# Kernel optimization log

Measured on AMD Instinct MI355X. Metric: run time of the kernel, lower is better.

Reference implementation:

```python
import jax, jax.numpy as jnp
import numpy as np
from jax.scipy.linalg import expm

B, HW, SPP, C, H, W = 4, 16384, 3, 64, 128, 128
D_SH = 25
EPS = 1e-8

# color SH mask: higher degrees downweighted (from GaussianAdapter.__init__)
_SH_MASK = np.ones(D_SH, np.float32)
for _d in range(1, 5):
    _SH_MASK[_d * _d:(_d + 1) * (_d + 1)] = 0.1 * 0.25 ** _d

# --- e3nn-style SO(3) generators for wigner_D (precomputed in numpy) ---

def _su2_generators(j):
    m = np.arange(-j, j)
    raising = np.diag(-np.sqrt(j * (j + 1) - m * (m + 1)), k=-1).astype(np.complex128)
    m = np.arange(-j + 1, j + 1)
    lowering = np.diag(np.sqrt(j * (j + 1) - m * (m - 1)), k=1).astype(np.complex128)
    m = np.arange(-j, j + 1)
    return np.stack([0.5 * (raising + lowering), np.diag(1j * m), -0.5j * (raising - lowering)])

def _change_basis(l):
    q = np.zeros((2 * l + 1, 2 * l + 1), dtype=np.complex128)
    for m in range(-l, 0):
        q[l + m, l + abs(m)] = 1 / np.sqrt(2)
        q[l + m, l - abs(m)] = -1j / np.sqrt(2)
    q[l, l] = 1.0
    for m in range(1, l + 1):
        q[l + m, l + abs(m)] = (-1) ** m / np.sqrt(2)
        q[l + m, l - abs(m)] = 1j * (-1) ** m / np.sqrt(2)
    return (-1j) ** l * q

def _so3_generators(l):
    X = _su2_generators(l)
    Q = _change_basis(l)
    return np.real(np.conj(Q.T) @ X @ Q).astype(np.float32)

_SO3 = [_so3_generators(l) for l in range(5)]

# --- small math helpers ---

def _quat_to_mat(q):  # q: (..., 4) wxyz, pytorch3d convention
    r, i, j, k = q[..., 0], q[..., 1], q[..., 2], q[..., 3]
    s = 2.0 / jnp.sum(q * q, axis=-1)
    m = jnp.stack([
        1 - s * (j * j + k * k), s * (i * j - k * r), s * (i * k + j * r),
        s * (i * j + k * r), 1 - s * (i * i + k * k), s * (j * k - i * r),
        s * (i * k - j * r), s * (j * k + i * r), 1 - s * (i * i + j * j)], -1)
    return m.reshape(q.shape[:-1] + (3, 3))

def _rot_y(a):
    c, s = jnp.cos(a), jnp.sin(a)
    z, o = jnp.zeros_like(a), jnp.ones_like(a)
    return jnp.stack([jnp.stack([c, z, s], -1), jnp.stack([z, o, z], -1), jnp.stack([-s, z, c], -1)], -2)

def _rot_x(a):
    c, s = jnp.cos(a), jnp.sin(a)
    z, o = jnp.zeros_like(a), jnp.ones_like(a)
    return jnp.stack([jnp.stack([o, z, z], -1), jnp.stack([z, c, -s], -1), jnp.stack([z, s, c], -1)], -2)

def _matrix_to_angles(R):  # e3nn matrix_to_angles, YXY convention
    x = R[..., :, 1]  # R @ e_y
    x = x / jnp.linalg.norm(x, axis=-1, keepdims=True)
    beta = jnp.arccos(jnp.clip(x[..., 1], -1.0, 1.0))
    alpha = jnp.arctan2(x[..., 0], x[..., 2])
    A = _rot_y(alpha) @ _rot_x(beta)  # angles_to_matrix(alpha, beta, 0)
    Rp = jnp.swapaxes(A, -1, -2) @ R
    gamma = jnp.arctan2(Rp[..., 0, 2], Rp[..., 0, 0])
    return alpha, beta, gamma

def _wigner_D(l, alpha, beta, gamma):  # alpha/beta/gamma: [b]
    X = jnp.asarray(_SO3[l])
    ea = jax.vmap(expm)(alpha[:, None, None] * X[1])
    eb = jax.vmap(expm)(beta[:, None, None] * X[0])
    eg = jax.vmap(expm)(gamma[:, None, None] * X[1])
    return ea @ eb @ eg  # [b, 2l+1, 2l+1]

def _rotate_sh(sh, R):  # sh: [b,hw,spp,3,25], R: [b,3,3]
    alpha, beta, gamma = _matrix_to_angles(R)
    out = []
    for l in range(5):
        D = _wigner_D(l, alpha, -beta, gamma)
        out.append(jnp.einsum('bij,bhscj->bhsci', D, sh[..., l * l:(l + 1) * (l + 1)]))
    return jnp.concatenate(out, axis=-1)

def _forward(extrinsics, intrinsics, coordinates, depths, opacities, raw_gaussians, grd_feat, image_h, image_w):
    scales_raw = raw_gaussians[..., :3]
    rot_raw = raw_gaussians[..., 3:7]
    color_sh = raw_gaussians[..., 7:7 + 3 * D_SH]
    b, c, h, w = grd_feat.shape
    features = jnp.transpose(grd_feat.reshape(b, c, h * w), (0, 2, 1))[:, :, None, :]  # [b,hw,1,c]
    scales = 0.5 + (15.0 - 0.5) * jax.nn.sigmoid(scales_raw)
    pixel_size = jnp.array([1.0 / image_w, 1.0 / image_h], dtype=jnp.float32)
    K2inv = jnp.linalg.inv(intrinsics[..., :2, :2])
    multiplier = 0.1 * jnp.einsum('bij,j->bi', K2inv, pixel_size).sum(-1)  # [b]
    scales = scales * depths[..., None] * multiplier[:, None, None, None]
    rotations = rot_raw / (jnp.linalg.norm(rot_raw, axis=-1, keepdims=True) + EPS)
    color_sh = color_sh.reshape(color_sh.shape[:-1] + (3, D_SH)) * jnp.asarray(_SH_MASK)
    features = jnp.broadcast_to(features, opacities.shape + (c,))
    # covariance = R S S^T R^T
    Rq = _quat_to_mat(rotations)
    covariances = jnp.einsum('...ij,...j,...kj->...ik', Rq, scales * scales, Rq)
    # world rays
    Kinv = jnp.linalg.inv(intrinsics)
    coords_h = jnp.concatenate([coordinates, jnp.ones_like(coordinates[..., :1])], -1)
    dirs = jnp.einsum('bij,bhsj->bhsi', Kinv, coords_h)
    dirs = dirs / jnp.linalg.norm(dirs, axis=-1, keepdims=True)
    Rc2w = extrinsics[..., :3, :3]
    dirs = jnp.einsum('bij,bhsj->bhsi', Rc2w, dirs)
    origins = extrinsics[:, None, None, :3, 3]
    means = origins + dirs * depths[..., None]
    sh_rot = _rotate_sh(color_sh, Rc2w)
    rotations = jnp.broadcast_to(rotations, scales.shape[:-1] + (4,))
    return (means, covariances, sh_rot, opacities, features, scales, rotations)

def setup_inputs() -> dict:
    key = jax.random.key(0)
    ks = jax.random.split(key, 8)
    q = jax.random.normal(ks[0], (B, 4), jnp.float32)
    q = q / jnp.linalg.norm(q, axis=-1, keepdims=True)
    R = _quat_to_mat(q)
    t = jax.random.normal(ks[1], (B, 3), jnp.float32)
    extrinsics = jnp.tile(jnp.eye(4, dtype=jnp.float32), (B, 1, 1)).at[:, :3, :3].set(R).at[:, :3, 3].set(t)
    f = jax.random.uniform(ks[2], (B, 2), jnp.float32, 0.4, 0.6)
    intrinsics = (jnp.zeros((B, 3, 3), jnp.float32)
                  .at[:, 0, 0].set(f[:, 0]).at[:, 1, 1].set(f[:, 1])
                  .at[:, 0, 2].set(0.5).at[:, 1, 2].set(0.5).at[:, 2, 2].set(1.0))
    coordinates = jax.random.uniform(ks[3], (B, HW, SPP, 2), jnp.float32)
    depths = jax.random.uniform(ks[4], (B, HW, SPP), jnp.float32) * 50.0 + 0.5
    opacities = jax.random.uniform(ks[5], (B, HW, SPP), jnp.float32)
    raw_gaussians = jax.random.normal(ks[6], (B, HW, SPP, 3 + 4 + 3 * D_SH), jnp.float32)
    grd_feat = jax.random.normal(ks[7], (B, C, H, W), jnp.float32)
    return {"extrinsics": extrinsics, "intrinsics": intrinsics, "coordinates": coordinates,
            "depths": depths, "opacities": opacities, "raw_gaussians": raw_gaussians,
            "grd_feat": grd_feat, "image_h": H, "image_w": W}

def reference(extrinsics, intrinsics, coordinates, depths, opacities, raw_gaussians, grd_feat, image_h, image_w):
    return _forward(extrinsics, intrinsics, coordinates, depths, opacities, raw_gaussians, grd_feat, image_h, image_w)
```

## Files before the change

kernel.cpp:

```cpp
#include <hip/hip_runtime.h>
#include <math.h>

#define N_TOT   196608
#define HWSPP   49152
#define RGF     82
#define RGS     83
#define NGB     3072
#define NFB     1024

#define OFF_MEANS 0
#define OFF_COV   589824
#define OFF_SH    2359296
#define OFF_OP    17104896
#define OFF_FEAT  17301504
#define OFF_SCL   29884416
#define OFF_ROT   30474240

__device__ __constant__ int c_loff[5] = {0, 1, 10, 35, 84};

__device__ __forceinline__ float sigmoidf_(float x) { return 1.0f / (1.0f + expf(-x)); }

__global__ __launch_bounds__(64) void setup_kernel(
    const float* __restrict__ extr, const float* __restrict__ intr,
    const int* __restrict__ img_h, const int* __restrict__ img_w,
    float* __restrict__ ws)
{
  const int b = blockIdx.x / 5;
  const int l = blockIdx.x % 5;
  const int n = 2 * l + 1;
  const int nn = n * n;
  const int t = threadIdx.x;

  __shared__ double Qr[81], Qi[81], X0c[81];
  __shared__ double X0r[81], U[9];
  __shared__ double A_[81], P0[81], P1[81], E0[81], E1[81];

  const float* Ex = extr + b * 16;
  double R00 = Ex[0], R01 = Ex[1], R02 = Ex[2];
  double R11 = Ex[5];
  double R20 = Ex[8], R21 = Ex[9], R22 = Ex[10];
  double x0 = R01, x1 = R11, x2 = R21;
  double nr = sqrt(x0 * x0 + x1 * x1 + x2 * x2);
  x0 /= nr; x1 /= nr; x2 /= nr;
  double beta  = acos(fmin(1.0, fmax(-1.0, x1)));
  double alpha = atan2(x0, x2);
  double ca_ = cos(alpha), sa_ = sin(alpha);
  double gamma = atan2(ca_ * R02 - sa_ * R22, ca_ * R00 - sa_ * R20);

  if (l == 0 && t == 0) {
    const float* K = intr + b * 9;
    double k00=K[0],k01=K[1],k02=K[2],k10=K[3],k11=K[4],k12=K[5],k20=K[6],k21=K[7],k22=K[8];
    double det = k00*(k11*k22-k12*k21) - k01*(k10*k22-k12*k20) + k02*(k10*k21-k11*k20);
    double id = 1.0 / det;
    float* kv = ws + 660 + b * 9;
    kv[0] = (float)((k11*k22-k12*k21)*id);
    kv[1] = (float)((k02*k21-k01*k22)*id);
    kv[2] = (float)((k01*k12-k02*k11)*id);
    kv[3] = (float)((k12*k20-k10*k22)*id);
    kv[4] = (float)((k00*k22-k02*k20)*id);
    kv[5] = (float)((k02*k10-k00*k12)*id);
    kv[6] = (float)((k10*k21-k11*k20)*id);
    kv[7] = (float)((k01*k20-k00*k21)*id);
    kv[8] = (float)((k00*k11-k01*k10)*id);
    double d2 = k00 * k11 - k01 * k10;
    double ps0 = 1.0 / (double)img_w[0];
    double ps1 = 1.0 / (double)img_h[0];
    double sum = (k11 * ps0 - k01 * ps1 - k10 * ps0 + k00 * ps1) / d2;
    ws[696 + b] = (float)(0.1 * sum);
  }

  for (int e = t; e < 81; e += 64) { Qr[e] = 0.0; Qi[e] = 0.0; X0c[e] = 0.0; }
  __syncthreads();
  if (t == 0) {
    const double irt2 = 0.70710678118654752440;
    for (int m = -l; m < 0; ++m) {
      Qr[(l + m) * n + (l - m)] = irt2;
      Qi[(l + m) * n + (l + m)] = -irt2;
    }
    Qr[l * n + l] = 1.0;
    for (int m = 1; m <= l; ++m) {
      double sg = (m & 1) ? -1.0 : 1.0;
      Qr[(l + m) * n + (l + m)] = sg * irt2;
      Qi[(l + m) * n + (l - m)] = sg * irt2;
    }
    for (int i = 0; i < n - 1; ++i) {
      double mi = (double)(-l + i);
      double ci = sqrt((double)(l * (l + 1)) - mi * (mi + 1.0));
      X0c[i * n + (i + 1)] = 0.5 * ci;
      X0c[(i + 1) * n + i] = -0.5 * ci;
    }
  }
  __syncthreads();
  for (int e = t; e < nn; e += 64) {
    int i = e / n, j = e % n; double s = 0, s2 = 0;
    for (int k = 0; k < n; ++k) { s += X0c[i*n+k]*Qr[k*n+j]; s2 += X0c[i*n+k]*Qi[k*n+j]; }
    P0[e] = s; P1[e] = s2;
  }
  __syncthreads();
  for (int e = t; e < nn; e += 64) {
    int a = e / n, c = e % n; double s = 0;
    for (int r = 0; r < n; ++r) s += Qr[r*n+a]*P0[r*n+c] + Qi[r*n+a]*P1[r*n+c];
    X0r[e] = s;
  }
  if (t < n) {
    int i = t, j = 2 * l - i; double s1 = 0;
    for (int r = 0; r < n; ++r) {
      double mr = (double)(r - l);
      s1 += mr * (Qi[r*n+i]*Qr[r*n+j] - Qr[r*n+i]*Qi[r*n+j]);
    }
    U[i] = s1;
  }
  __syncthreads();

  const double ths = -beta / 64.0;
  for (int e = t; e < nn; e += 64) { A_[e] = ths * X0r[e]; P0[e] = A_[e]; }
  double Ereg[2];
  {
    int ii = 0;
    for (int e = t; e < nn; e += 64) { Ereg[ii++] = ((e/n)==(e%n) ? 1.0 : 0.0) + ths * X0r[e]; }
  }
  __syncthreads();
  double* Pc = P0; double* Pn = P1;
  for (int k = 2; k <= 12; ++k) {
    int ii = 0;
    for (int e = t; e < nn; e += 64) {
      int i = e / n, j = e % n; double s = 0;
      for (int kk = 0; kk < n; ++kk) s += Pc[i*n+kk] * A_[kk*n+j];
      s /= (double)k;
      Pn[e] = s; Ereg[ii++] += s;
    }
    __syncthreads();
    double* tmp = Pc; Pc = Pn; Pn = tmp;
  }
  {
    int ii = 0;
    for (int e = t; e < nn; e += 64) E0[e] = Ereg[ii++];
  }
  __syncthreads();
  double* Es = E0; double* Ed = E1;
  for (int q = 0; q < 6; ++q) {
    for (int e = t; e < nn; e += 64) {
      int i = e / n, j = e % n; double s = 0;
      for (int kk = 0; kk < n; ++kk) s += Es[i*n+kk] * Es[kk*n+j];
      Ed[e] = s;
    }
    __syncthreads();
    double* tmp = Es; Es = Ed; Ed = tmp;
  }

  for (int e = t; e < nn; e += 64) {
    int i = e / n, j = e % n;
    int i2 = 2 * l - i, j2 = 2 * l - j;
    double cai = cos(alpha * U[i]), sai = sin(alpha * U[i]);
    double cgj = cos(gamma * U[j]), sgj = sin(gamma * U[j]);
    double w1 = cgj * Es[i *n + j] - sgj * Es[i *n + j2];
    double w2 = cgj * Es[i2*n + j] - sgj * Es[i2*n + j2];
    ws[b * 165 + c_loff[l] + e] = (float)(cai * w1 + sai * w2);
  }
}

__global__ __launch_bounds__(256) void main_kernel(
    const float* __restrict__ extr,
    const float* __restrict__ coords,
    const float* __restrict__ depths,
    const float* __restrict__ opac,
    const float* __restrict__ rg,
    const float* __restrict__ gf,
    const float* __restrict__ ws,
    float* __restrict__ out)
{
  __shared__ __align__(16) float smem[11584];
  const int t = threadIdx.x;

  if (blockIdx.x >= NGB) {
    float* tile = smem;
    const int blk = blockIdx.x - NGB;
    const int b = blk >> 8;
    const int hw0 = (blk & 255) << 6;
    const int tx = t & 63, ty = t >> 6;
    const float* src = gf + (size_t)b * 64 * 16384 + hw0;
#pragma unroll
    for (int i = 0; i < 16; ++i) {
      int c = i * 4 + ty;
      tile[c * 65 + tx] = src[(size_t)c * 16384 + tx];
    }
    __syncthreads();
    float* dst = out + OFF_FEAT + ((size_t)(b * 16384 + hw0)) * 3 * 64;
    for (int r = ty; r < 192; r += 4) {
      int hw = r / 3;
      dst[(size_t)r * 64 + tx] = tile[tx * 65 + hw];
    }
    return;
  }

  float* sIn    = smem;
  float* sSh    = smem + 5312;
  float* sSmall = smem + 10112;
  float* sD     = smem + 11392;
  float* sKinv  = smem + 11557;
  float* sRc    = smem + 11566;
  float* sOrig  = smem + 11575;
  float* sMult  = smem + 11578;

  const int g0 = blockIdx.x * 64;
  const int b  = g0 / HWSPP;

  if (t < 165) sD[t] = ws[b * 165 + t];
  else if (t < 174) sKinv[t - 165] = ws[660 + b * 9 + (t - 165)];
  else if (t < 183) { int k = t - 174; sRc[k] = extr[b * 16 + (k / 3) * 4 + (k % 3)]; }
  else if (t < 186) sOrig[t - 183] = extr[b * 16 + (t - 183) * 4 + 3];
  else if (t == 186) sMult[0] = ws[696 + b];

  {
    const float4* src4 = (const float4*)(rg + (size_t)g0 * RGF);
    for (int idx = t; idx < (64 * RGF) / 4; idx += 256) {
      float4 v = src4[idx];
      int base = idx * 4;
      int gg = base / RGF;
      int ff = base - gg * RGF;
      float vv[4] = {v.x, v.y, v.z, v.w};
#pragma unroll
      for (int e = 0; e < 4; ++e) {
        int g2 = gg, f2 = ff + e;
        if (f2 >= RGF) { g2 += 1; f2 -= RGF; }
        sIn[g2 * RGS + f2] = vv[e];
      }
    }
  }
  __syncthreads();

  if (t < 64) {
    const int gidx = g0 + t;
    const float* q = &sIn[t * RGS];
    const float dpt = depths[gidx];
    const float mlt = sMult[0];
    float sc0 = (0.5f + 14.5f * sigmoidf_(q[0])) * dpt * mlt;
    float sc1 = (0.5f + 14.5f * sigmoidf_(q[1])) * dpt * mlt;
    float sc2 = (0.5f + 14.5f * sigmoidf_(q[2])) * dpt * mlt;
    float r0 = q[3], r1 = q[4], r2 = q[5], r3 = q[6];
    float nr = sqrtf(r0*r0 + r1*r1 + r2*r2 + r3*r3) + 1e-8f;
    float qr = r0/nr, qi = r1/nr, qj = r2/nr, qk = r3/nr;
    float s2 = 2.0f / (qr*qr + qi*qi + qj*qj + qk*qk);
    float R00 = 1.0f - s2*(qj*qj + qk*qk);
    float R01 = s2*(qi*qj - qk*qr);
    float R02 = s2*(qi*qk + qj*qr);
    float R10 = s2*(qi*qj + qk*qr);
    float R11 = 1.0f - s2*(qi*qi + qk*qk);
    float R12 = s2*(qj*qk - qi*qr);
    float R20 = s2*(qi*qk - qj*qr);
    float R21 = s2*(qj*qk + qi*qr);
    float R22 = 1.0f - s2*(qi*qi + qj*qj);
    float v0 = sc0*sc0, v1 = sc1*sc1, v2 = sc2*sc2;
    float C00 = R00*R00*v0 + R01*R01*v1 + R02*R02*v2;
    float C01 = R00*R10*v0 + R01*R11*v1 + R02*R12*v2;
    float C02 = R00*R20*v0 + R01*R21*v1 + R02*R22*v2;
    float C11 = R10*R10*v0 + R11*R11*v1 + R12*R12*v2;
    float C12 = R10*R20*v0 + R11*R21*v1 + R12*R22*v2;
    float C22 = R20*R20*v0 + R21*R21*v1 + R22*R22*v2;
    float2 cxy = ((const float2*)coords)[gidx];
    float dx = sKinv[0]*cxy.x + sKinv[1]*cxy.y + sKinv[2];
    float dy = sKinv[3]*cxy.x + sKinv[4]*cxy.y + sKinv[5];
    float dz = sKinv[6]*cxy.x + sKinv[7]*cxy.y + sKinv[8];
    float inr = 1.0f / sqrtf(dx*dx + dy*dy + dz*dz);
    dx *= inr; dy *= inr; dz *= inr;
    float wx = sRc[0]*dx + sRc[1]*dy + sRc[2]*dz;
    float wy = sRc[3]*dx + sRc[4]*dy + sRc[5]*dz;
    float wz = sRc[6]*dx + sRc[7]*dy + sRc[8]*dz;
    sSmall[t*3+0] = sOrig[0] + wx * dpt;
    sSmall[t*3+1] = sOrig[1] + wy * dpt;
    sSmall[t*3+2] = sOrig[2] + wz * dpt;
    float* cc = &sSmall[192 + t*9];
    cc[0]=C00; cc[1]=C01; cc[2]=C02; cc[3]=C01; cc[4]=C11; cc[5]=C12; cc[6]=C02; cc[7]=C12; cc[8]=C22;
    float* ss = &sSmall[768 + t*3]; ss[0]=sc0; ss[1]=sc1; ss[2]=sc2;
    float* rr = &sSmall[960 + t*4]; rr[0]=qr; rr[1]=qi; rr[2]=qj; rr[3]=qk;
    sSmall[1216 + t] = opac[gidx];
  } else {
    const int task = t - 64;
    const int gg = task & 63;
    const int ch = task >> 6;
    const float* shin = &sIn[gg * RGS + 7 + ch * 25];
    float* shout = &sSh[gg * 75 + ch * 25];
    float in_[25];
#pragma unroll
    for (int j = 0; j < 25; ++j) in_[j] = shin[j];
    shout[0] = sD[0] * in_[0];
#pragma unroll
    for (int i = 0; i < 3; ++i) {
      float a = sD[1+i*3]*in_[1] + sD[1+i*3+1]*in_[2] + sD[1+i*3+2]*in_[3];
      shout[1 + i] = (float)(0.1 * 0.25) * a;
    }
#pragma unroll
    for (int i = 0; i < 5; ++i) {
      float a = 0.f;
#pragma unroll
      for (int j = 0; j < 5; ++j) a += sD[10 + i*5 + j] * in_[4 + j];
      shout[4 + i] = (float)(0.1 * 0.0625) * a;
    }
#pragma unroll
    for (int i = 0; i < 7; ++i) {
      float a = 0.f;
#pragma unroll
      for (int j = 0; j < 7; ++j) a += sD[35 + i*7 + j] * in_[9 + j];
      shout[9 + i] = (float)(0.1 * 0.015625) * a;
    }
#pragma unroll
    for (int i = 0; i < 9; ++i) {
      float a = 0.f;
#pragma unroll
      for (int j = 0; j < 9; ++j) a += sD[84 + i*9 + j] * in_[16 + j];
      shout[16 + i] = (float)(0.1 * 0.00390625) * a;
    }
  }
  __syncthreads();

  {
    float4* osh = (float4*)(out + OFF_SH + (size_t)g0 * 75);
    const float4* s4 = (const float4*)sSh;
    for (int idx = t; idx < 1200; idx += 256) osh[idx] = s4[idx];
    float* om  = out + OFF_MEANS + (size_t)g0 * 3;
    float* oc  = out + OFF_COV   + (size_t)g0 * 9;
    float* os  = out + OFF_SCL   + (size_t)g0 * 3;
    float* orr = out + OFF_ROT   + (size_t)g0 * 4;
    float* oo  = out + OFF_OP    + (size_t)g0;
    if (t < 192) { om[t] = sSmall[t]; os[t] = sSmall[768 + t]; }
    for (int idx = t; idx < 576; idx += 256) oc[idx] = sSmall[192 + idx];
    orr[t] = sSmall[960 + t];
    if (t < 64) oo[t] = sSmall[1216 + t];
  }
}

extern "C" void kernel_launch(void* const* d_in, const int* in_sizes, int n_in,
                              void* d_out, int out_size, void* d_ws, size_t ws_size,
                              hipStream_t stream)
{
  const float* extr   = (const float*)d_in[0];
  const float* intr   = (const float*)d_in[1];
  const float* coords = (const float*)d_in[2];
  const float* depths = (const float*)d_in[3];
  const float* opac   = (const float*)d_in[4];
  const float* rg     = (const float*)d_in[5];
  const float* gf     = (const float*)d_in[6];
  const int*   ih     = (const int*)d_in[7];
  const int*   iw     = (const int*)d_in[8];
  float* out = (float*)d_out;
  float* ws  = (float*)d_ws;

  hipLaunchKernelGGL(setup_kernel, dim3(20), dim3(64), 0, stream, extr, intr, ih, iw, ws);
  hipLaunchKernelGGL(main_kernel, dim3(NGB + NFB), dim3(256), 0, stream,
                     extr, coords, depths, opac, rg, gf, ws, out);
}
```

Baseline: 243.8 us.

## Shrink shared memory by reusing input buffer and interleave transpose blocks

Shared memory per block drops from about 46KB to 27KB by loading inputs into registers, adding a barrier, and writing SH outputs back into the input buffer. Launch bounds now request 6 blocks per CU, and the feature-transpose blocks are interleaved with gaussian blocks (every 4th block) instead of appended at the end. Per-gaussian scalar loads (depth, opacity, coords) are hoisted before the barrier so their latency overlaps the bulk load. The aim is higher occupancy and better mixing of memory-bound work, at the cost of an extra barrier and more register pressure under the occupancy hint.

```diff
diff --git a/kernel.cpp b/kernel.cpp
--- a/kernel.cpp
+++ b/kernel.cpp
@@ -159,7 +159,7 @@
   }
 }
 
-__global__ __launch_bounds__(256) void main_kernel(
+__global__ __launch_bounds__(256, 6) void main_kernel(
     const float* __restrict__ extr,
     const float* __restrict__ coords,
     const float* __restrict__ depths,
@@ -169,14 +169,15 @@
     const float* __restrict__ ws,
     float* __restrict__ out)
 {
-  __shared__ __align__(16) float smem[11584];
+  __shared__ __align__(16) float smem[6784];
   const int t = threadIdx.x;
-
-  if (blockIdx.x >= NGB) {
+  const int bq = blockIdx.x >> 2;
+  const int br = blockIdx.x & 3;
+
+  if (br == 3) {
     float* tile = smem;
-    const int blk = blockIdx.x - NGB;
-    const int b = blk >> 8;
-    const int hw0 = (blk & 255) << 6;
+    const int b = bq >> 8;
+    const int hw0 = (bq & 255) << 6;
     const int tx = t & 63, ty = t >> 6;
     const float* src = gf + (size_t)b * 64 * 16384 + hw0;
 #pragma unroll
@@ -193,17 +194,26 @@
     return;
   }
 
+  const int gb = bq * 3 + br;
   float* sIn    = smem;
-  float* sSh    = smem + 5312;
-  float* sSmall = smem + 10112;
-  float* sD     = smem + 11392;
-  float* sKinv  = smem + 11557;
-  float* sRc    = smem + 11566;
-  float* sOrig  = smem + 11575;
-  float* sMult  = smem + 11578;
-
-  const int g0 = blockIdx.x * 64;
+  float* sSmall = smem + 5312;
+  float* sD     = smem + 6592;
+  float* sKinv  = smem + 6757;
+  float* sRc    = smem + 6766;
+  float* sOrig  = smem + 6775;
+  float* sMult  = smem + 6778;
+
+  const int g0 = gb * 64;
   const int b  = g0 / HWSPP;
+
+  float dpt = 0.f, opc = 0.f;
+  float2 cxy = make_float2(0.f, 0.f);
+  if (t < 64) {
+    const int gidx = g0 + t;
+    dpt = depths[gidx];
+    opc = opac[gidx];
+    cxy = ((const float2*)coords)[gidx];
+  }
 
   if (t < 165) sD[t] = ws[b * 165 + t];
   else if (t < 174) sKinv[t - 165] = ws[660 + b * 9 + (t - 165)];
@@ -229,15 +239,28 @@
   }
   __syncthreads();
 
+  float reg[25];
+  int gg = 0, ch = 0;
   if (t < 64) {
-    const int gidx = g0 + t;
     const float* q = &sIn[t * RGS];
-    const float dpt = depths[gidx];
+#pragma unroll
+    for (int j = 0; j < 7; ++j) reg[j] = q[j];
+  } else {
+    const int task = t - 64;
+    gg = task & 63;
+    ch = task >> 6;
+    const float* shin = &sIn[gg * RGS + 7 + ch * 25];
+#pragma unroll
+    for (int j = 0; j < 25; ++j) reg[j] = shin[j];
+  }
+  __syncthreads();
+
+  if (t < 64) {
     const float mlt = sMult[0];
-    float sc0 = (0.5f + 14.5f * sigmoidf_(q[0])) * dpt * mlt;
-    float sc1 = (0.5f + 14.5f * sigmoidf_(q[1])) * dpt * mlt;
-    float sc2 = (0.5f + 14.5f * sigmoidf_(q[2])) * dpt * mlt;
-    float r0 = q[3], r1 = q[4], r2 = q[5], r3 = q[6];
+    float sc0 = (0.5f + 14.5f * sigmoidf_(reg[0])) * dpt * mlt;
+    float sc1 = (0.5f + 14.5f * sigmoidf_(reg[1])) * dpt * mlt;
+    float sc2 = (0.5f + 14.5f * sigmoidf_(reg[2])) * dpt * mlt;
+    float r0 = reg[3], r1 = reg[4], r2 = reg[5], r3 = reg[6];
     float nr = sqrtf(r0*r0 + r1*r1 + r2*r2 + r3*r3) + 1e-8f;
     float qr = r0/nr, qi = r1/nr, qj = r2/nr, qk = r3/nr;
     float s2 = 2.0f / (qr*qr + qi*qi + qj*qj + qk*qk);
@@ -257,7 +280,6 @@
     float C11 = R10*R10*v0 + R11*R11*v1 + R12*R12*v2;
     float C12 = R10*R20*v0 + R11*R21*v1 + R12*R22*v2;
     float C22 = R20*R20*v0 + R21*R21*v1 + R22*R22*v2;
-    float2 cxy = ((const float2*)coords)[gidx];
     float dx = sKinv[0]*cxy.x + sKinv[1]*cxy.y + sKinv[2];
     float dy = sKinv[3]*cxy.x + sKinv[4]*cxy.y + sKinv[5];
     float dz = sKinv[6]*cxy.x + sKinv[7]*cxy.y + sKinv[8];
@@ -273,41 +295,34 @@
     cc[0]=C00; cc[1]=C01; cc[2]=C02; cc[3]=C01; cc[4]=C11; cc[5]=C12; cc[6]=C02; cc[7]=C12; cc[8]=C22;
     float* ss = &sSmall[768 + t*3]; ss[0]=sc0; ss[1]=sc1; ss[2]=sc2;
     float* rr = &sSmall[960 + t*4]; rr[0]=qr; rr[1]=qi; rr[2]=qj; rr[3]=qk;
-    sSmall[1216 + t] = opac[gidx];
+    sSmall[1216 + t] = opc;
   } else {
-    const int task = t - 64;
-    const int gg = task & 63;
-    const int ch = task >> 6;
-    const float* shin = &sIn[gg * RGS + 7 + ch * 25];
-    float* shout = &sSh[gg * 75 + ch * 25];
-    float in_[25];
-#pragma unroll
-    for (int j = 0; j < 25; ++j) in_[j] = shin[j];
-    shout[0] = sD[0] * in_[0];
+    float* shout = &sIn[gg * 75 + ch * 25];
+    shout[0] = sD[0] * reg[0];
 #pragma unroll
     for (int i = 0; i < 3; ++i) {
-      float a = sD[1+i*3]*in_[1] + sD[1+i*3+1]*in_[2] + sD[1+i*3+2]*in_[3];
+      float a = sD[1+i*3]*reg[1] + sD[1+i*3+1]*reg[2] + sD[1+i*3+2]*reg[3];
       shout[1 + i] = (float)(0.1 * 0.25) * a;
     }
 #pragma unroll
     for (int i = 0; i < 5; ++i) {
       float a = 0.f;
 #pragma unroll
-      for (int j = 0; j < 5; ++j) a += sD[10 + i*5 + j] * in_[4 + j];
+      for (int j = 0; j < 5; ++j) a += sD[10 + i*5 + j] * reg[4 + j];
       shout[4 + i] = (float)(0.1 * 0.0625) * a;
     }
 #pragma unroll
     for (int i = 0; i < 7; ++i) {
       float a = 0.f;
 #pragma unroll
-      for (int j = 0; j < 7; ++j) a += sD[35 + i*7 + j] * in_[9 + j];
+      for (int j = 0; j < 7; ++j) a += sD[35 + i*7 + j] * reg[9 + j];
       shout[9 + i] = (float)(0.1 * 0.015625) * a;
     }
 #pragma unroll
     for (int i = 0; i < 9; ++i) {
       float a = 0.f;
 #pragma unroll
-      for (int j = 0; j < 9; ++j) a += sD[84 + i*9 + j] * in_[16 + j];
+      for (int j = 0; j < 9; ++j) a += sD[84 + i*9 + j] * reg[16 + j];
       shout[16 + i] = (float)(0.1 * 0.00390625) * a;
     }
   }
@@ -315,7 +330,7 @@
 
   {
     float4* osh = (float4*)(out + OFF_SH + (size_t)g0 * 75);
-    const float4* s4 = (const float4*)sSh;
+    const float4* s4 = (const float4*)sIn;
     for (int idx = t; idx < 1200; idx += 256) osh[idx] = s4[idx];
     float* om  = out + OFF_MEANS + (size_t)g0 * 3;
     float* oc  = out + OFF_COV   + (size_t)g0 * 9;
```

Result: faster. 236.9 us (-2.8%).
